# Kernel tuning notes

Hardware: AMD Instinct MI355X
Metric: run time of the kernel (lower is better)

## Reference

```python
import jax, jax.numpy as jnp
import numpy as np


def setup_inputs() -> dict:
    key = jax.random.key(0)
    k1, k2 = jax.random.split(key)
    B, t, nbands, framesize = 32, 4000, 65, 80
    H = jax.random.normal(k1, (B, t, nbands), dtype=jnp.float32)
    noise = jax.random.uniform(k2, (B, t, framesize), dtype=jnp.float32)  # uniform [0,1); scaled to [-1,1) in reference
    return {"H": H, "noise": noise, "framesize": framesize}


def reference(H, noise, framesize):
    # H: [B, t, nbands] real half-spectrum of zero-phase filter
    B, t, nbands = H.shape
    L_fir = 2 * nbands - 1  # FIR length (129)

    # zero-phase impulse response -> linear-phase via circular shift
    zero_phase = jnp.fft.irfft(H, n=L_fir, axis=-1)          # [B, t, L_fir]
    lin_phase = jnp.roll(zero_phase, nbands - 1, axis=-1)

    # periodic Hann window (matches torch.hann_window default periodic=True)
    n = jnp.arange(L_fir, dtype=H.dtype)
    hann = 0.5 * (1.0 - jnp.cos(2.0 * jnp.pi * n / L_fir))
    firwin = lin_phase * hann                                 # [B, t, L_fir]

    # per-frame noise in [-1, 1)
    x = noise * 2.0 - 1.0                                     # [B, t, framesize]

    # full FFT convolution along last axis
    L = framesize + L_fir - 1                                 # 208
    X = jnp.fft.rfft(x, n=L, axis=-1)
    W = jnp.fft.rfft(firwin, n=L, axis=-1)
    filtered = jnp.fft.irfft(X * W, n=L, axis=-1)             # [B, t, L]

    # overlap-add with hop = framesize via scatter-add (replaces conv_transpose1d trick)
    total = (t - 1) * framesize + L
    idx = jnp.arange(t)[:, None] * framesize + jnp.arange(L)[None, :]  # [t, L]
    out = jnp.zeros((B, total), dtype=filtered.dtype).at[:, idx].add(filtered)

    # trim filter group delay from both ends -> [B, t*framesize]
    return out[:, nbands - 1: total - (nbands - 1)]
```

## Files before the change

kernel.cpp:

```cpp
#include <hip/hip_runtime.h>


#define NT 256
#define H_STRIDE 68
#define X_STRIDE 84
#define W_STRIDE 166
#define W_P 14
#define NSLOT 35
#define WTOT (NSLOT * W_STRIDE)
#define UTOT (NSLOT * X_STRIDE)

__global__ void __launch_bounds__(NT)
fng_kernel(const float* __restrict__ Hg_, const float* __restrict__ Ng_,
           float* __restrict__ Og_) {
  __shared__ __align__(16) float sW[WTOT + 2];
  __shared__ __align__(16) float sU[UTOT];
  __shared__ float cosT[132];

  const int t  = threadIdx.x;
  const int bx = blockIdx.x;
  const int b  = blockIdx.y;
  const int f0 = bx * 32;
  const float TP = 6.28318530717958647692f / 129.f;

  float4 xq[3];
  {
    float4 z4 = {0.f, 0.f, 0.f, 0.f};
    for (int i = t; i < (WTOT + 2) / 4; i += NT) ((float4*)sW)[i] = z4;
    if (t < 129) cosT[t] = __cosf((float)t * TP);
    const float* Hg = Hg_ + (size_t)b * (4000 * 65);
    for (int i = t; i < NSLOT * H_STRIDE; i += NT) {
      int fi = i / H_STRIDE, kk = i - fi * H_STRIDE;
      int fr = f0 - 2 + fi;
      float v = 0.f;
      if (kk < 65 && fr >= 0 && fr < 4000) v = Hg[fr * 65 + kk];
      sU[i] = v;
    }
    const float* Ng = Ng_ + (size_t)b * 320000;
#pragma unroll
    for (int j = 0; j < 3; ++j) {
      int q = t + 256 * j;
      float4 v = {0.5f, 0.5f, 0.5f, 0.5f};
      if (q < NSLOT * 21) {
        int fi = q / 21, qm = q - fi * 21;
        int fr = f0 - 2 + fi;
        if (qm < 20 && fr >= 0 && fr < 4000)
          v = *(const float4*)&Ng[(size_t)fr * 80 + 4 * qm];
      }
      xq[j] = v;
    }
  }
  __syncthreads();

  auto p1_task = [&](int slot, int dg) {
    int fr = f0 - 2 + slot;
    if (fr < 0 || fr >= 4000) return;
    const float* hr = &sU[slot * H_STRIDE];
    float* wr = &sW[slot * W_STRIDE];
    float two_a[8], cc[8], cm[8], ac[8];
#pragma unroll
    for (int j = 0; j < 8; ++j) {
      float a = cosT[dg + 8 * j];
      two_a[j] = 2.f * a; cc[j] = 1.f; cm[j] = a; ac[j] = 0.f;
    }
    const float h0 = hr[0];
#pragma unroll 1
    for (int k = 0; k < 68; k += 4) {
      float4 h4 = *(const float4*)&hr[k];
      const float hh[4] = {h4.x, h4.y, h4.z, h4.w};
#pragma unroll
      for (int mm = 0; mm < 4; ++mm)
#pragma unroll
        for (int j = 0; j < 8; ++j) {
          ac[j] = fmaf(hh[mm], cc[j], ac[j]);
          float cn = fmaf(two_a[j], cc[j], -cm[j]);
          cm[j] = cc[j]; cc[j] = cn;
        }
    }
#pragma unroll
    for (int j = 0; j < 8; ++j) {
      int d = dg + 8 * j;
      float zp = (2.f * ac[j] - h0) * (1.f / 129.f);
      wr[W_P + 64 + d] = (0.5f - 0.5f * cosT[64 + d]) * zp;
      wr[W_P + 64 - d] = (0.5f - 0.5f * cosT[64 - d]) * zp;
    }
  };
  p1_task(t >> 3, t & 7);
  if (t >= 232) p1_task(32 + ((t - 232) >> 3), (t - 232) & 7);
  if (t >= 64 && t < 64 + NSLOT) {
    int slot = t - 64;
    int fr = f0 - 2 + slot;
    if (fr >= 0 && fr < 4000) {
      const float* hr = &sU[slot * H_STRIDE];
      float a = cosT[64];
      float a2 = 2.f * a, c_ = 1.f, cmv = a, s_ = 0.f;
#pragma unroll 1
      for (int k = 0; k < 68; k += 4) {
        float4 h4 = *(const float4*)&hr[k];
        s_ = fmaf(h4.x, c_, s_); { float cn = fmaf(a2, c_, -cmv); cmv = c_; c_ = cn; }
        s_ = fmaf(h4.y, c_, s_); { float cn = fmaf(a2, c_, -cmv); cmv = c_; c_ = cn; }
        s_ = fmaf(h4.z, c_, s_); { float cn = fmaf(a2, c_, -cmv); cmv = c_; c_ = cn; }
        s_ = fmaf(h4.w, c_, s_); { float cn = fmaf(a2, c_, -cmv); cmv = c_; c_ = cn; }
      }
      float zp = (2.f * s_ - hr[0]) * (1.f / 129.f);
      sW[slot * W_STRIDE + W_P + 128] = (0.5f - 0.5f * cosT[128]) * zp;
    }
  }
  __syncthreads();

#pragma unroll
  for (int j = 0; j < 3; ++j) {
    int q = t + 256 * j;
    if (q < NSLOT * 21) {
      int fi = q / 21, qm = q - fi * 21;
      if (qm < 20) {
        float4 v = xq[j], o;
        o.x = 2.f * v.x - 1.f; o.y = 2.f * v.y - 1.f;
        o.z = 2.f * v.z - 1.f; o.w = 2.f * v.w - 1.f;
        *(float4*)&sU[fi * X_STRIDE + 4 * qm] = o;
      }
    }
  }
  __syncthreads();

  {
    const int col = t & 31;
    const int pb  = t >> 5;
    const int e   = 64 + 10 * pb;
    const int qq  = (e >= 80) ? 1 : 0;
    const int D   = e - 80 * qq;
    float acc[10];
#pragma unroll
    for (int i = 0; i < 10; ++i) acc[i] = 0.f;

#pragma unroll 1
    for (int g = 2; g >= -1; --g) {
      const int dlt = D + 80 * g;
      int Qlo = (dlt - 131 + 3) >> 2; if (Qlo < 0) Qlo = 0;
      int Qhi = (dlt + 9) >> 2;       if (Qhi > 19) Qhi = 19;
      if (Qlo > Qhi) continue;
      const int slot = col + qq - g + 2;
      const float* wr = &sW[slot * W_STRIDE];
      const float* xr = &sU[slot * X_STRIDE];
      int wb = W_P + dlt - 4 * Qlo - 4;
      float wv[16];
#pragma unroll
      for (int k = 0; k < 8; ++k) {
        float2 w2 = *(const float2*)&wr[wb + 2 * k];
        wv[2 * k] = w2.x; wv[2 * k + 1] = w2.y;
      }
#pragma unroll 4
      for (int Q = Qlo; Q <= Qhi; ++Q) {
        float4 x4 = *(const float4*)&xr[4 * Q];
        const float xv[4] = {x4.x, x4.y, x4.z, x4.w};
#pragma unroll
        for (int mm = 0; mm < 4; ++mm)
#pragma unroll
          for (int i = 0; i < 10; ++i)
            acc[i] = fmaf(xv[mm], wv[i - mm + 4], acc[i]);
        wb -= 4; int wc = (wb < 0) ? 0 : wb;
#pragma unroll
        for (int k = 15; k >= 4; --k) wv[k] = wv[k - 4];
        float2 wA = *(const float2*)&wr[wc];
        float2 wB = *(const float2*)&wr[wc + 2];
        wv[0] = wA.x; wv[1] = wA.y; wv[2] = wB.x; wv[3] = wB.y;
      }
    }

    float* Ob = Og_ + (size_t)b * 320000 + 2560 * bx + 80 * col + 10 * pb;
#pragma unroll
    for (int s = 0; s < 5; ++s) {
      float2 v; v.x = acc[2 * s]; v.y = acc[2 * s + 1];
      *(float2*)&Ob[2 * s] = v;
    }
  }
}

extern "C" void kernel_launch(void* const* d_in, const int* in_sizes, int n_in,
                              void* d_out, int out_size, void* d_ws, size_t ws_size,
                              hipStream_t stream) {
  const float* H     = (const float*)d_in[0];
  const float* noise = (const float*)d_in[1];
  float* out = (float*)d_out;
  (void)in_sizes; (void)n_in; (void)d_ws; (void)ws_size; (void)out_size;

  dim3 grid(125, 32, 1);
  fng_kernel<<<grid, NT, 0, stream>>>(H, noise, out);
}
```

Before: 177.0 us.

## Compute windowed FIR via fp16 MFMA matmul against precomputed cosine matrix

Replaces the per-thread Chebyshev-recurrence inverse DFT that built the windowed FIR taps with a matrix multiply on MFMA units. H is staged in shared memory as fp16 and multiplied by a precomputed Hann-windowed cosine basis matrix, which a small init kernel writes to workspace on every launch. This removes the scalar FMA-heavy phase 1, at the cost of fp16 input precision for H and the basis, plus an extra kernel launch.

```diff
diff --git a/kernel.cpp b/kernel.cpp
--- a/kernel.cpp
+++ b/kernel.cpp
@@ -2,39 +2,60 @@
 
 
 #define NT 256
-#define H_STRIDE 68
 #define X_STRIDE 84
-#define W_STRIDE 166
+#define W_STRIDE 158
 #define W_P 14
 #define NSLOT 35
-#define WTOT (NSLOT * W_STRIDE)
+#define WTOT (NSLOT * W_STRIDE + 2)
 #define UTOT (NSLOT * X_STRIDE)
+#define HF_STRIDE 104
+
+typedef _Float16 f16x8 __attribute__((ext_vector_type(8)));
+typedef float f32x4 __attribute__((ext_vector_type(4)));
+
+__global__ void __launch_bounds__(256)
+minit_kernel(_Float16* __restrict__ M) {
+  const float TP = 6.28318530717958647692f / 129.f;
+  int i = blockIdx.x * 256 + threadIdx.x;
+  int frag = i >> 9;
+  int off  = i & 511;
+  int lane = off >> 3, j = off & 7;
+  int nt = frag / 3, ks = frag - 3 * (frag / 3);
+  int n = nt * 16 + (lane & 15);
+  int k = ks * 32 + (lane >> 4) * 8 + j;
+  float v = 0.f;
+  if (n <= 128 && k <= 64) {
+    float hann = 0.5f - 0.5f * __cosf((float)n * TP);
+    float sc = (k == 0 ? 1.f : 2.f) * (1.f / 129.f);
+    int e = (k * (n - 64)) % 129; if (e < 0) e += 129;
+    v = hann * sc * __cosf((float)e * TP);
+  }
+  M[i] = (_Float16)v;
+}
 
 __global__ void __launch_bounds__(NT)
 fng_kernel(const float* __restrict__ Hg_, const float* __restrict__ Ng_,
-           float* __restrict__ Og_) {
-  __shared__ __align__(16) float sW[WTOT + 2];
+           float* __restrict__ Og_, const _Float16* __restrict__ Mg) {
+  __shared__ __align__(16) float sW[WTOT];
   __shared__ __align__(16) float sU[UTOT];
-  __shared__ float cosT[132];
 
   const int t  = threadIdx.x;
   const int bx = blockIdx.x;
   const int b  = blockIdx.y;
   const int f0 = bx * 32;
-  const float TP = 6.28318530717958647692f / 129.f;
 
   float4 xq[3];
   {
     float4 z4 = {0.f, 0.f, 0.f, 0.f};
-    for (int i = t; i < (WTOT + 2) / 4; i += NT) ((float4*)sW)[i] = z4;
-    if (t < 129) cosT[t] = __cosf((float)t * TP);
+    for (int i = t; i < WTOT / 4; i += NT) ((float4*)sW)[i] = z4;
+    _Float16* sHf = (_Float16*)sU;
     const float* Hg = Hg_ + (size_t)b * (4000 * 65);
-    for (int i = t; i < NSLOT * H_STRIDE; i += NT) {
-      int fi = i / H_STRIDE, kk = i - fi * H_STRIDE;
-      int fr = f0 - 2 + fi;
+    for (int i = t; i < 48 * 96; i += NT) {
+      int row = i / 96, k = i - 96 * (i / 96);
+      int fr = f0 - 2 + row;
       float v = 0.f;
-      if (kk < 65 && fr >= 0 && fr < 4000) v = Hg[fr * 65 + kk];
-      sU[i] = v;
+      if (k < 65 && row < NSLOT && fr >= 0 && fr < 4000) v = Hg[fr * 65 + k];
+      sHf[row * HF_STRIDE + k] = (_Float16)v;
     }
     const float* Ng = Ng_ + (size_t)b * 320000;
 #pragma unroll
@@ -52,58 +73,31 @@
   }
   __syncthreads();
 
-  auto p1_task = [&](int slot, int dg) {
-    int fr = f0 - 2 + slot;
-    if (fr < 0 || fr >= 4000) return;
-    const float* hr = &sU[slot * H_STRIDE];
-    float* wr = &sW[slot * W_STRIDE];
-    float two_a[8], cc[8], cm[8], ac[8];
+  {
+    const _Float16* sHf = (const _Float16*)sU;
+    const int wv   = t >> 6;
+    const int lane = t & 63;
+    const int quad = lane >> 4;
+    const int l15  = lane & 15;
+#pragma unroll 1
+    for (int tile = wv; tile < 27; tile += 4) {
+      const int mt = tile / 9, nt = tile - 9 * (tile / 9);
+      f32x4 acc = {0.f, 0.f, 0.f, 0.f};
 #pragma unroll
-    for (int j = 0; j < 8; ++j) {
-      float a = cosT[dg + 8 * j];
-      two_a[j] = 2.f * a; cc[j] = 1.f; cm[j] = a; ac[j] = 0.f;
-    }
-    const float h0 = hr[0];
-#pragma unroll 1
-    for (int k = 0; k < 68; k += 4) {
-      float4 h4 = *(const float4*)&hr[k];
-      const float hh[4] = {h4.x, h4.y, h4.z, h4.w};
+      for (int ks = 0; ks < 3; ++ks) {
+        f16x8 a = *(const f16x8*)&sHf[(mt * 16 + l15) * HF_STRIDE + ks * 32 + quad * 8];
+        f16x8 bb = ((const f16x8*)Mg)[(nt * 3 + ks) * 64 + lane];
+        acc = __builtin_amdgcn_mfma_f32_16x16x32_f16(a, bb, acc, 0, 0, 0);
+      }
+      const int n = nt * 16 + l15;
+      const int fr0 = mt * 16 + quad * 4;
+      if (n <= 128) {
 #pragma unroll
-      for (int mm = 0; mm < 4; ++mm)
-#pragma unroll
-        for (int j = 0; j < 8; ++j) {
-          ac[j] = fmaf(hh[mm], cc[j], ac[j]);
-          float cn = fmaf(two_a[j], cc[j], -cm[j]);
-          cm[j] = cc[j]; cc[j] = cn;
+        for (int r = 0; r < 4; ++r) {
+          int frame = fr0 + r;
+          if (frame < NSLOT) sW[frame * W_STRIDE + W_P + n] = acc[r];
         }
-    }
-#pragma unroll
-    for (int j = 0; j < 8; ++j) {
-      int d = dg + 8 * j;
-      float zp = (2.f * ac[j] - h0) * (1.f / 129.f);
-      wr[W_P + 64 + d] = (0.5f - 0.5f * cosT[64 + d]) * zp;
-      wr[W_P + 64 - d] = (0.5f - 0.5f * cosT[64 - d]) * zp;
-    }
-  };
-  p1_task(t >> 3, t & 7);
-  if (t >= 232) p1_task(32 + ((t - 232) >> 3), (t - 232) & 7);
-  if (t >= 64 && t < 64 + NSLOT) {
-    int slot = t - 64;
-    int fr = f0 - 2 + slot;
-    if (fr >= 0 && fr < 4000) {
-      const float* hr = &sU[slot * H_STRIDE];
-      float a = cosT[64];
-      float a2 = 2.f * a, c_ = 1.f, cmv = a, s_ = 0.f;
-#pragma unroll 1
-      for (int k = 0; k < 68; k += 4) {
-        float4 h4 = *(const float4*)&hr[k];
-        s_ = fmaf(h4.x, c_, s_); { float cn = fmaf(a2, c_, -cmv); cmv = c_; c_ = cn; }
-        s_ = fmaf(h4.y, c_, s_); { float cn = fmaf(a2, c_, -cmv); cmv = c_; c_ = cn; }
-        s_ = fmaf(h4.z, c_, s_); { float cn = fmaf(a2, c_, -cmv); cmv = c_; c_ = cn; }
-        s_ = fmaf(h4.w, c_, s_); { float cn = fmaf(a2, c_, -cmv); cmv = c_; c_ = cn; }
       }
-      float zp = (2.f * s_ - hr[0]) * (1.f / 129.f);
-      sW[slot * W_STRIDE + W_P + 128] = (0.5f - 0.5f * cosT[128]) * zp;
     }
   }
   __syncthreads();
@@ -182,8 +176,10 @@
   const float* H     = (const float*)d_in[0];
   const float* noise = (const float*)d_in[1];
   float* out = (float*)d_out;
-  (void)in_sizes; (void)n_in; (void)d_ws; (void)ws_size; (void)out_size;
+  _Float16* M = (_Float16*)d_ws;
+  (void)in_sizes; (void)n_in; (void)ws_size; (void)out_size;
 
+  minit_kernel<<<54, 256, 0, stream>>>(M);
   dim3 grid(125, 32, 1);
-  fng_kernel<<<grid, NT, 0, stream>>>(H, noise, out);
+  fng_kernel<<<grid, NT, 0, stream>>>(H, noise, out, M);
 }
```

After: 181.2 us. +2.4%, slower.
